# Performance work log

Hardware: AMD Instinct MI355X
Metric: run time of the kernel (lower is better)

The kernel has to match this reference:

```python
import jax, jax.numpy as jnp
import numpy as np

B, D, H, N, M, K = 128, 256, 4, 256, 256, 10  # M=256 is hardcoded in the original repeat(1,1,1,256)
DIM = D // H  # per-head dim = 64


def setup_inputs() -> dict:
    key = jax.random.key(0)
    ks = jax.random.split(key, 10)
    s = 0.05  # weight scale
    return {
        "x": jax.random.normal(ks[0], (B, D, N), jnp.float32),
        "source": jax.random.normal(ks[1], (B, D, M), jnp.float32),
        "Wq": jax.random.normal(ks[2], (D, D), jnp.float32) * s,
        "bq": jax.random.normal(ks[3], (D,), jnp.float32) * s,
        "Wk": jax.random.normal(ks[4], (D, D), jnp.float32) * s,
        "bk": jax.random.normal(ks[5], (D,), jnp.float32) * s,
        "Wv": jax.random.normal(ks[6], (D, D), jnp.float32) * s,
        "bv": jax.random.normal(ks[7], (D,), jnp.float32) * s,
        "Wm": jax.random.normal(ks[8], (D, D), jnp.float32) * s,
        "bm": jax.random.normal(ks[9], (D,), jnp.float32) * s,
        "k": K,
    }


def _pointwise(W, b, x):
    # nn.Conv1d(d, d, kernel_size=1): per-point linear over channel dim
    return jnp.einsum('ef,bfn->ben', W, x) + b[None, :, None]


def reference(x, source, Wq, bq, Wk, bk, Wv, bv, Wm, bm, k):
    b, d, n = x.shape
    # torch .view(b, dim, heads, -1) splits channels as (dim, heads)
    q = _pointwise(Wq, bq, x).reshape(b, DIM, H, n)
    kk = _pointwise(Wk, bk, source).reshape(b, DIM, H, -1)
    v = _pointwise(Wv, bv, source).reshape(b, DIM, H, -1)

    scores = jnp.einsum('bdhn,bdhm->bhnm', q, kk) / jnp.sqrt(jnp.asarray(DIM, x.dtype))
    # per-row top-k threshold: keep only scores >= k-th largest, softmax over kept
    thresh = jax.lax.top_k(scores, k)[0][..., k - 1:k]  # [b,h,n,1]
    mask = scores >= thresh
    neg = jnp.finfo(scores.dtype).min
    prob = jax.nn.softmax(jnp.where(mask, scores, neg), axis=-1)
    prob = jnp.where(mask, prob, jnp.zeros((), scores.dtype))

    out = jnp.einsum('bhnm,bdhm->bdhn', prob, v).reshape(b, d, n)
    return _pointwise(Wm, bm, out)
```

## Files before the change

kernel.cpp:

```cpp
#include <hip/hip_runtime.h>
#include <hip/hip_bf16.h>

#define BB   128
#define DDIM 256
#define HH   4
#define NNN  256
#define MMM  256

typedef __hip_bfloat16 bf16;
typedef short  short8   __attribute__((ext_vector_type(8)));
typedef unsigned short ushort8_t __attribute__((ext_vector_type(8)));
typedef float  f32x4    __attribute__((ext_vector_type(4)));
typedef float  f32x2    __attribute__((ext_vector_type(2)));

__device__ __forceinline__ unsigned short f2bf(float x) {
    unsigned u = __builtin_bit_cast(unsigned, x);
    u += 0x7FFFu + ((u >> 16) & 1u);
    return (unsigned short)(u >> 16);
}
__device__ __forceinline__ float bf2f(unsigned short b) {
    unsigned u = ((unsigned)b) << 16;
    return __builtin_bit_cast(float, u);
}

__device__ __forceinline__ void xpose4(float v[4], const int p) {
    float ta = __shfl_xor((p & 1) ? v[0] : v[1], 1, 64);
    float tb = __shfl_xor((p & 1) ? v[2] : v[3], 1, 64);
    float u0 = (p & 1) ? ta : v[0];
    float u1 = (p & 1) ? v[1] : ta;
    float u2 = (p & 1) ? tb : v[2];
    float u3 = (p & 1) ? v[3] : tb;
    float tc = __shfl_xor((p & 2) ? u0 : u2, 2, 64);
    float td = __shfl_xor((p & 2) ? u1 : u3, 2, 64);
    v[0] = (p & 2) ? tc : u0;
    v[1] = (p & 2) ? td : u1;
    v[2] = (p & 2) ? u2 : tc;
    v[3] = (p & 2) ? u3 : td;
}

__device__ __forceinline__ void split3_store8k(char* dst, const float v[4]) {
    unsigned short h[4], m[4], l[4];
    #pragma unroll
    for (int i = 0; i < 4; ++i) {
        h[i] = f2bf(v[i]);
        float r1 = v[i] - bf2f(h[i]);
        m[i] = f2bf(r1);
        float r2 = r1 - bf2f(m[i]);
        l[i] = f2bf(r2);
    }
    uint2 hp, mp, lp;
    hp.x = (unsigned)h[0] | ((unsigned)h[1] << 16);
    hp.y = (unsigned)h[2] | ((unsigned)h[3] << 16);
    mp.x = (unsigned)m[0] | ((unsigned)m[1] << 16);
    mp.y = (unsigned)m[2] | ((unsigned)m[3] << 16);
    lp.x = (unsigned)l[0] | ((unsigned)l[1] << 16);
    lp.y = (unsigned)l[2] | ((unsigned)l[3] << 16);
    *(uint2*)dst = hp;
    *(uint2*)(dst + 8192) = mp;
    *(uint2*)(dst + 16384) = lp;
}

__device__ __forceinline__ void split2_store(char* dst, const float v[4]) {
    unsigned short h[4], m[4];
    #pragma unroll
    for (int i = 0; i < 4; ++i) {
        h[i] = f2bf(v[i]);
        float r1 = v[i] - bf2f(h[i]);
        m[i] = f2bf(r1);
    }
    uint2 hp, mp;
    hp.x = (unsigned)h[0] | ((unsigned)h[1] << 16);
    hp.y = (unsigned)h[2] | ((unsigned)h[3] << 16);
    mp.x = (unsigned)m[0] | ((unsigned)m[1] << 16);
    mp.y = (unsigned)m[2] | ((unsigned)m[3] << 16);
    *(uint2*)dst = hp;
    *(uint2*)(dst + 16384) = mp;
}

__device__ __forceinline__ void ldx4(const float* p, float v[4]) {
    const float4 f = *(const float4*)p;
    v[0] = f.x; v[1] = f.y; v[2] = f.z; v[3] = f.w;
}
__device__ __forceinline__ void ldx4(const bf16* p, float v[4]) {
    uint2 u = *(const uint2*)p;
    v[0] = bf2f((unsigned short)(u.x & 0xFFFF));
    v[1] = bf2f((unsigned short)(u.x >> 16));
    v[2] = bf2f((unsigned short)(u.y & 0xFFFF));
    v[3] = bf2f((unsigned short)(u.y >> 16));
}

__device__ __forceinline__ float max16v(const float* w) {
    float a = fmaxf(fmaxf(w[0], w[1]),  fmaxf(w[2], w[3]));
    float b = fmaxf(fmaxf(w[4], w[5]),  fmaxf(w[6], w[7]));
    float c = fmaxf(fmaxf(w[8], w[9]),  fmaxf(w[10], w[11]));
    float d = fmaxf(fmaxf(w[12], w[13]), fmaxf(w[14], w[15]));
    return fmaxf(fmaxf(a, b), fmaxf(c, d));
}
__device__ __forceinline__ float gmax16(float v) {
    v = fmaxf(v, __shfl_xor(v, 1, 64));
    v = fmaxf(v, __shfl_xor(v, 2, 64));
    v = fmaxf(v, __shfl_xor(v, 4, 64));
    v = fmaxf(v, __shfl_xor(v, 8, 64));
    return v;
}
__device__ __forceinline__ float gsum16(float v) {
    v += __shfl_xor(v, 1, 64);
    v += __shfl_xor(v, 2, 64);
    v += __shfl_xor(v, 4, 64);
    v += __shfl_xor(v, 8, 64);
    return v;
}

template <int MODE>
__global__ __launch_bounds__(256)
void projqk_kernel(const float* __restrict__ X, const float* __restrict__ W,
                   const float* __restrict__ bias, float* __restrict__ Yt,
                   unsigned short* __restrict__ Ph, unsigned short* __restrict__ Pm,
                   unsigned short* __restrict__ Pl) {
    __shared__ float Wt[32][268];
    __shared__ float Xt[32][36];

    const int t  = threadIdx.x;
    const int tx = t & 7;
    const int ty = t >> 3;
    const int n0 = blockIdx.x * 32;
    const int b  = blockIdx.y;
    const size_t plane = (size_t)b * DDIM * NNN;

    f32x2 acc2[8][2];
    #pragma unroll
    for (int i = 0; i < 8; ++i) {
        acc2[i][0] = f32x2{0.f, 0.f};
        acc2[i][1] = f32x2{0.f, 0.f};
    }

    for (int f0 = 0; f0 < DDIM; f0 += 32) {
        #pragma unroll
        for (int i = 0; i < 8; ++i) {
            int idx = t + i * 256;
            int fq = idx & 7, el = idx >> 3;
            const float4 w4 = *(const float4*)&W[(size_t)el * DDIM + f0 + fq * 4];
            Wt[fq * 4 + 0][el] = w4.x;
            Wt[fq * 4 + 1][el] = w4.y;
            Wt[fq * 4 + 2][el] = w4.z;
            Wt[fq * 4 + 3][el] = w4.w;
        }
        #pragma unroll
        for (int i = 0; i < 4; ++i) {
            int idx = t + i * 256;
            int fl = idx >> 5, nl = idx & 31;
            Xt[fl][nl] = X[plane + (size_t)(f0 + fl) * NNN + n0 + nl];
        }
        __syncthreads();

        #pragma unroll
        for (int ff = 0; ff < 32; ++ff) {
            const float4 av0 = *(const float4*)&Wt[ff][ty * 8];
            const float4 av1 = *(const float4*)&Wt[ff][ty * 8 + 4];
            const float4 bv  = *(const float4*)&Xt[ff][tx * 4];
            const float a[8] = {av0.x, av0.y, av0.z, av0.w, av1.x, av1.y, av1.z, av1.w};
            const f32x2 c0 = {bv.x, bv.y};
            const f32x2 c1 = {bv.z, bv.w};
            #pragma unroll
            for (int i2 = 0; i2 < 8; ++i2) {
                const f32x2 aa = {a[i2], a[i2]};
                acc2[i2][0] = __builtin_elementwise_fma(aa, c0, acc2[i2][0]);
                acc2[i2][1] = __builtin_elementwise_fma(aa, c1, acc2[i2][1]);
            }
        }
        __syncthreads();
    }

    float* stage = &Wt[0][0];
    #pragma unroll
    for (int i2 = 0; i2 < 8; ++i2) {
        const int e = ty * 8 + i2;
        const float bs = bias[e];
        const int col = (e & 3) * 64 + (e >> 2);
        stage[(tx * 4 + 0) * 260 + col] = acc2[i2][0].x + bs;
        stage[(tx * 4 + 1) * 260 + col] = acc2[i2][0].y + bs;
        stage[(tx * 4 + 2) * 260 + col] = acc2[i2][1].x + bs;
        stage[(tx * 4 + 3) * 260 + col] = acc2[i2][1].y + bs;
    }
    __syncthreads();

    #pragma unroll
    for (int it = 0; it < 8; ++it) {
        int gid = t + it * 256;
        int n   = gid >> 6;
        int sub = gid & 63;
        const float4 v4 = *(const float4*)&stage[n * 260 + sub * 4];
        const int hh = sub >> 4;
        const int dd0 = (sub & 15) * 4;
        const size_t off = ((size_t)(b * 4 + hh) * NNN + n0 + n) * 64 + dd0;
        if constexpr (MODE == 0) {
            *(float4*)&Yt[off] = v4;
        } else {
            const float v[4] = {v4.x, v4.y, v4.z, v4.w};
            unsigned short h[4], m[4], l[4];
            #pragma unroll
            for (int i = 0; i < 4; ++i) {
                h[i] = f2bf(v[i]);
                float r1 = v[i] - bf2f(h[i]);
                m[i] = f2bf(r1);
                float r2 = r1 - bf2f(m[i]);
                l[i] = f2bf(r2);
            }
            uint2 hp, mp, lp;
            hp.x = (unsigned)h[0] | ((unsigned)h[1] << 16);
            hp.y = (unsigned)h[2] | ((unsigned)h[3] << 16);
            mp.x = (unsigned)m[0] | ((unsigned)m[1] << 16);
            mp.y = (unsigned)m[2] | ((unsigned)m[3] << 16);
            lp.x = (unsigned)l[0] | ((unsigned)l[1] << 16);
            lp.y = (unsigned)l[2] | ((unsigned)l[3] << 16);
            *(uint2*)&Ph[off] = hp;
            *(uint2*)&Pm[off] = mp;
            *(uint2*)&Pl[off] = lp;
        }
    }
}

__global__ __launch_bounds__(256, 4)
void attn4_kernel(const float* __restrict__ qt,
                  const unsigned short* __restrict__ khp,
                  const unsigned short* __restrict__ kmp,
                  const unsigned short* __restrict__ klp,
                  const bf16* __restrict__ vb, bf16* __restrict__ ob,
                  const int* __restrict__ kptr) {
    extern __shared__ __align__(16) char smem[];

    const int t    = threadIdx.x;
    const int lane = t & 63;
    const int w    = t >> 6;
    const int g    = lane >> 4;
    const int c16  = lane & 15;

    const int i    = blockIdx.x;
    const int work = (i & 7) * 256 + (i >> 3);
    const int bx = work & 3;
    const int h  = (work >> 2) & 3;
    const int b  = work >> 4;
    const int n0 = bx * 64;
    const int bh = b * 4 + h;

    const size_t planeV = (size_t)b * DDIM * MMM;

    int kk = kptr[0];
    kk = kk < 1 ? 1 : (kk > MMM ? MMM : kk);

    #pragma unroll
    for (int it = 0; it < 4; ++it) {
        int gid = t + it * 256;
        int dq = gid & 15;
        int n  = gid >> 4;
        const float4 q4 = *(const float4*)&qt[((size_t)bh * NNN + n0 + n) * 64 + dq * 4];
        float v[4] = {q4.x * 0.125f, q4.y * 0.125f, q4.z * 0.125f, q4.w * 0.125f};
        int base = n * 128 + ((dq * 8) ^ ((n & 7) << 4));
        split3_store8k(smem + base, v);
    }
    __syncthreads();

    short8 qh[2], qm[2], ql[2];
    #pragma unroll
    for (int ks = 0; ks < 2; ++ks) {
        int nl = w * 16 + c16;
        int off = nl * 128 + ((ks * 64 + g * 16) ^ ((nl & 7) << 4));
        qh[ks] = *(const short8*)(smem + off);
        qm[ks] = *(const short8*)(smem + 8192 + off);
        ql[ks] = *(const short8*)(smem + 16384 + off);
    }
    __syncthreads();

    f32x4 acc[16];
    #pragma unroll
    for (int m = 0; m < 16; ++m) acc[m] = f32x4{0.f, 0.f, 0.f, 0.f};

    #pragma unroll
    for (int tt = 0; tt < 4; ++tt) {
        if (tt) __syncthreads();
        #pragma unroll
        for (int it = 0; it < 6; ++it) {
            int gid = t + it * 256;
            int pl  = gid >> 9;
            int rem = gid & 511;
            int ml  = rem >> 3;
            int dq  = rem & 7;
            int dqs = dq ^ (ml & 7);
            const unsigned short* kp = (pl == 0) ? khp : (pl == 1 ? kmp : klp);
            const unsigned short* src = kp + ((size_t)bh * MMM + tt * 64 + ml) * 64 + dqs * 8;
            __builtin_amdgcn_global_load_lds(
                (const __attribute__((address_space(1))) void*)src,
                (__attribute__((address_space(3))) void*)(smem + gid * 16),
                16, 0, 0);
        }
        __syncthreads();

        #pragma unroll
        for (int mf = 0; mf < 4; ++mf) {
            #pragma unroll
            for (int ks = 0; ks < 2; ++ks) {
                int ml = mf * 16 + c16;
                int off = ml * 128 + ((ks * 64 + g * 16) ^ ((ml & 7) << 4));
                short8 bh_ = *(const short8*)(smem + off);
                short8 bm_ = *(const short8*)(smem + 8192 + off);
                short8 bl_ = *(const short8*)(smem + 16384 + off);
                f32x4 a = acc[tt * 4 + mf];
                a = __builtin_amdgcn_mfma_f32_16x16x32_bf16(qh[ks], bh_, a, 0, 0, 0);
                a = __builtin_amdgcn_mfma_f32_16x16x32_bf16(qh[ks], bm_, a, 0, 0, 0);
                a = __builtin_amdgcn_mfma_f32_16x16x32_bf16(qm[ks], bh_, a, 0, 0, 0);
                a = __builtin_amdgcn_mfma_f32_16x16x32_bf16(qm[ks], bm_, a, 0, 0, 0);
                a = __builtin_amdgcn_mfma_f32_16x16x32_bf16(qh[ks], bl_, a, 0, 0, 0);
                a = __builtin_amdgcn_mfma_f32_16x16x32_bf16(ql[ks], bh_, a, 0, 0, 0);
                acc[tt * 4 + mf] = a;
            }
        }
    }
    __syncthreads();

    float thr[4], rmx[4];
    #pragma unroll
    for (int r = 0; r < 4; ++r) {
        float w16[16];
        #pragma unroll
        for (int mf = 0; mf < 16; ++mf) w16[mf] = acc[mf][r];
        float lm = max16v(w16);
        float gm = gmax16(lm);
        rmx[r] = gm;
        for (int it = 1; it < kk; ++it) {
            unsigned long long bal = __ballot(lm == gm);
            unsigned gmask = (unsigned)((bal >> (g * 16)) & 0xFFFFull);
            int leader = __builtin_ctz(gmask);
            bool skip = (c16 != leader);
            #pragma unroll
            for (int mf = 0; mf < 16; ++mf) {
                bool hit = (!skip) && (w16[mf] == gm);
                w16[mf] = hit ? -INFINITY : w16[mf];
                skip = skip || hit;
            }
            lm = max16v(w16);
            gm = gmax16(lm);
        }
        thr[r] = gm;
    }

    #pragma unroll
    for (int mf = 0; mf < 16; ++mf) {
        #pragma unroll
        for (int r = 0; r < 4; ++r) {
            float a = acc[mf][r];
            acc[mf][r] = (a >= thr[r]) ? __expf(a - rmx[r]) : 0.f;
        }
    }
    float inv_[4];
    #pragma unroll
    for (int r = 0; r < 4; ++r) {
        float s = ((acc[0][r] + acc[1][r]) + (acc[2][r] + acc[3][r]))
                + ((acc[4][r] + acc[5][r]) + (acc[6][r] + acc[7][r]))
                + ((acc[8][r] + acc[9][r]) + (acc[10][r] + acc[11][r]))
                + ((acc[12][r] + acc[13][r]) + (acc[14][r] + acc[15][r]));
        s = gsum16(s);
        inv_[r] = 1.0f / s;
    }
    #pragma unroll
    for (int mf = 0; mf < 16; ++mf) {
        #pragma unroll
        for (int r = 0; r < 4; ++r) {
            int row = w * 16 + g * 4 + r;
            int m2  = (mf * 16 + c16) * 2;
            int off = row * 512 + (m2 ^ ((row & 7) << 4));
            *(unsigned short*)(smem + off) = f2bf(acc[mf][r] * inv_[r]);
        }
    }
    __syncthreads();

    f32x4 o[4];
    #pragma unroll
    for (int df = 0; df < 4; ++df) o[df] = f32x4{0.f, 0.f, 0.f, 0.f};

    #pragma unroll
    for (int half = 0; half < 2; ++half) {
        short8 pa[4];
        #pragma unroll
        for (int ks = 0; ks < 4; ++ks) {
            int row = w * 16 + c16;
            int off = row * 512 + ((half * 256 + ks * 64 + g * 16) ^ ((row & 7) << 4));
            pa[ks] = *(const short8*)(smem + off);
        }
        #pragma unroll
        for (int df = 0; df < 4; ++df) {
            int d = df * 16 + c16;
            const bf16* vrow = vb + planeV + (size_t)(d * HH + h) * MMM + half * 128;
            f32x4 o_ = o[df];
            #pragma unroll
            for (int ks = 0; ks < 4; ++ks) {
                short8 vv = *(const short8*)(vrow + ks * 32 + g * 8);
                o_ = __builtin_amdgcn_mfma_f32_16x16x32_bf16(pa[ks], vv, o_, 0, 0, 0);
            }
            o[df] = o_;
        }
    }
    __syncthreads();

    #pragma unroll
    for (int df = 0; df < 4; ++df)
        #pragma unroll
        for (int r = 0; r < 4; ++r) {
            int d  = df * 16 + c16;
            int nl = w * 16 + g * 4 + r;
            int off = d * 128 + ((nl * 2) ^ ((d & 7) << 4));
            *(unsigned short*)(smem + off) = f2bf(o[df][r]);
        }
    __syncthreads();
    #pragma unroll
    for (int it = 0; it < 2; ++it) {
        int idx = t + it * 256;
        int d = idx >> 3, ch = idx & 7;
        int off = d * 128 + ((ch * 16) ^ ((d & 7) << 4));
        ushort8_t val = *(const ushort8_t*)(smem + off);
        *(ushort8_t*)&ob[planeV + (size_t)(d * HH + h) * NNN + n0 + ch * 8] = val;
    }
}

template <typename TIN, typename TOUT>
__global__ __launch_bounds__(512, 2)
void projm_kernel(const TIN* __restrict__ X, const float* __restrict__ W,
                  const float* __restrict__ bias, TOUT* __restrict__ Y) {
    extern __shared__ __align__(16) char smem[];

    const int t    = threadIdx.x;
    const int lane = t & 63;
    const int w    = t >> 6;
    const int c16  = lane & 15;
    const int g    = (lane >> 4) & 3;
    const int p    = lane & 3;
    const int G    = lane >> 2;

    const int n0 = blockIdx.x * 128;
    const int e0 = blockIdx.y * 128;
    const int b  = blockIdx.z;
    const size_t plane = (size_t)b * DDIM * NNN;

    f32x4 acc[8];
    #pragma unroll
    for (int nf = 0; nf < 8; ++nf) acc[nf] = f32x4{0.f, 0.f, 0.f, 0.f};

    #pragma unroll
    for (int ft = 0; ft < 4; ++ft) {
        const int f0 = ft * 64;
        if (ft) __syncthreads();
        #pragma unroll
        for (int it = 0; it < 4; ++it) {
            int chunk = w + 8 * it;
            int fch = chunk & 15, nh = chunk >> 4;
            float v[4];
            ldx4(&X[plane + (size_t)(f0 + fch * 4 + p) * NNN + n0 + nh * 64 + G * 4], v);
            xpose4(v, p);
            int nl = nh * 64 + G * 4 + p;
            int base = nl * 128 + ((fch * 8) ^ ((nl & 7) << 4));
            split2_store(smem + base, v);
        }
        #pragma unroll
        for (int it = 0; it < 4; ++it) {
            int idx = t + 512 * it;
            int el = idx >> 4, fq = idx & 15;
            float v[4];
            const float4 f4 = *(const float4*)&W[(size_t)(e0 + el) * DDIM + f0 + fq * 4];
            v[0] = f4.x; v[1] = f4.y; v[2] = f4.z; v[3] = f4.w;
            int base = 32768 + el * 128 + ((fq * 8) ^ ((el & 7) << 4));
            split2_store(smem + base, v);
        }
        __syncthreads();

        const int ew = w * 16;
        short8 a0[2], a1[2];
        #pragma unroll
        for (int ks = 0; ks < 2; ++ks) {
            int off = 32768 + (ew + c16) * 128
                    + ((ks * 64 + g * 16) ^ ((c16 & 7) << 4));
            a0[ks] = *(const short8*)(smem + off);
            a1[ks] = *(const short8*)(smem + off + 16384);
        }
        #pragma unroll
        for (int nf = 0; nf < 8; ++nf) {
            #pragma unroll
            for (int ks = 0; ks < 2; ++ks) {
                int off = (nf * 16 + c16) * 128
                        + ((ks * 64 + g * 16) ^ ((c16 & 7) << 4));
                short8 b0 = *(const short8*)(smem + off);
                short8 b1 = *(const short8*)(smem + off + 16384);
                f32x4 a = acc[nf];
                a = __builtin_amdgcn_mfma_f32_16x16x32_bf16(a0[ks], b0, a, 0, 0, 0);
                a = __builtin_amdgcn_mfma_f32_16x16x32_bf16(a0[ks], b1, a, 0, 0, 0);
                a = __builtin_amdgcn_mfma_f32_16x16x32_bf16(a1[ks], b0, a, 0, 0, 0);
                acc[nf] = a;
            }
        }
    }

    const int ew = w * 16;
    float bs[4];
    #pragma unroll
    for (int r = 0; r < 4; ++r) bs[r] = bias[e0 + ew + g * 4 + r];
    #pragma unroll
    for (int nf = 0; nf < 8; ++nf) {
        #pragma unroll
        for (int r = 0; r < 4; ++r) {
            size_t off = plane + (size_t)(e0 + ew + g * 4 + r) * NNN + n0 + nf * 16 + c16;
            float val = acc[nf][r] + bs[r];
            if constexpr (sizeof(TOUT) == 4) Y[off] = val;
            else                             *(unsigned short*)&Y[off] = f2bf(val);
        }
    }
}

extern "C" void kernel_launch(void* const* d_in, const int* in_sizes, int n_in,
                              void* d_out, int out_size, void* d_ws, size_t ws_size,
                              hipStream_t stream) {
    const float* x   = (const float*)d_in[0];
    const float* src = (const float*)d_in[1];
    const float* Wq  = (const float*)d_in[2];
    const float* bq  = (const float*)d_in[3];
    const float* Wk  = (const float*)d_in[4];
    const float* bk  = (const float*)d_in[5];
    const float* Wv  = (const float*)d_in[6];
    const float* bv  = (const float*)d_in[7];
    const float* Wm  = (const float*)d_in[8];
    const float* bm  = (const float*)d_in[9];
    const int*   kp  = (const int*)d_in[10];
    float* out = (float*)d_out;

    char* ws = (char*)d_ws;
    const size_t QT_BYTES = 33554432;
    const size_t PL_BYTES = 16777216;

    float*          qt = (float*)(ws);
    unsigned short* kh = (unsigned short*)(ws + QT_BYTES);
    unsigned short* km = (unsigned short*)(ws + QT_BYTES + PL_BYTES);
    unsigned short* kl = (unsigned short*)(ws + QT_BYTES + 2 * PL_BYTES);
    bf16*           vb = (bf16*)(ws + QT_BYTES + 3 * PL_BYTES);
    bf16*           ob = (bf16*)(ws + QT_BYTES + 4 * PL_BYTES);

    hipFuncSetAttribute((const void*)(projm_kernel<float, bf16>),
                        hipFuncAttributeMaxDynamicSharedMemorySize, 65536);
    hipFuncSetAttribute((const void*)(projm_kernel<bf16, float>),
                        hipFuncAttributeMaxDynamicSharedMemorySize, 65536);
    hipFuncSetAttribute((const void*)attn4_kernel,
                        hipFuncAttributeMaxDynamicSharedMemorySize, 32768);

    dim3 qk_grid(NNN / 32, BB);
    dim3 mgrid(2, 2, BB);

    hipLaunchKernelGGL((projqk_kernel<0>), qk_grid, dim3(256), 0, stream,
                       x,   Wq, bq, qt, nullptr, nullptr, nullptr);
    hipLaunchKernelGGL((projqk_kernel<1>), qk_grid, dim3(256), 0, stream,
                       src, Wk, bk, nullptr, kh, km, kl);
    hipLaunchKernelGGL((projm_kernel<float, bf16>), mgrid, dim3(512), 65536, stream,
                       src, Wv, bv, vb);
    hipLaunchKernelGGL(attn4_kernel, dim3(2048), dim3(256), 32768, stream,
                       qt, kh, km, kl, vb, ob, kp);
    hipLaunchKernelGGL((projm_kernel<bf16, float>), mgrid, dim3(512), 65536, stream,
                       ob, Wm, bm, out);
}
```

Measured before the change: 289.9 us.

## Retile Q/K projection, drop redundant split term for bf16 input in output projection

Retiles the fp32 Q/K projection kernel from 256x32 tiles to 128x128 output tiles per block, giving more register reuse per shared-memory load and moving shared memory to dynamic allocation. The output projection with bf16 input no longer splits the input into high and low bf16 parts, since the low part is always zero. This removes one MFMA and one LDS read per step and shrinks shared memory. It also raises the attention kernel's occupancy hint to 5 and restructures max16v. The larger Q/K tiles use more registers per thread, which may limit occupancy.

```diff
diff --git a/kernel.cpp b/kernel.cpp
--- a/kernel.cpp
+++ b/kernel.cpp
@@ -77,6 +77,13 @@
     *(uint2*)(dst + 16384) = mp;
 }
 
+__device__ __forceinline__ void split1_store(char* dst, const float v[4]) {
+    uint2 hp;
+    hp.x = (unsigned)f2bf(v[0]) | ((unsigned)f2bf(v[1]) << 16);
+    hp.y = (unsigned)f2bf(v[2]) | ((unsigned)f2bf(v[3]) << 16);
+    *(uint2*)dst = hp;
+}
+
 __device__ __forceinline__ void ldx4(const float* p, float v[4]) {
     const float4 f = *(const float4*)p;
     v[0] = f.x; v[1] = f.y; v[2] = f.z; v[3] = f.w;
@@ -90,11 +97,14 @@
 }
 
 __device__ __forceinline__ float max16v(const float* w) {
-    float a = fmaxf(fmaxf(w[0], w[1]),  fmaxf(w[2], w[3]));
-    float b = fmaxf(fmaxf(w[4], w[5]),  fmaxf(w[6], w[7]));
-    float c = fmaxf(fmaxf(w[8], w[9]),  fmaxf(w[10], w[11]));
-    float d = fmaxf(fmaxf(w[12], w[13]), fmaxf(w[14], w[15]));
-    return fmaxf(fmaxf(a, b), fmaxf(c, d));
+    float a = fmaxf(fmaxf(w[0],  w[1]),  w[2]);
+    float b = fmaxf(fmaxf(w[3],  w[4]),  w[5]);
+    float c = fmaxf(fmaxf(w[6],  w[7]),  w[8]);
+    float d = fmaxf(fmaxf(w[9],  w[10]), w[11]);
+    float e = fmaxf(fmaxf(w[12], w[13]), w[14]);
+    float ab = fmaxf(fmaxf(a, b), c);
+    float de = fmaxf(fmaxf(d, e), w[15]);
+    return fmaxf(ab, de);
 }
 __device__ __forceinline__ float gmax16(float v) {
     v = fmaxf(v, __shfl_xor(v, 1, 64));
@@ -112,57 +122,62 @@
 }
 
 template <int MODE>
-__global__ __launch_bounds__(256)
+__global__ __launch_bounds__(256, 4)
 void projqk_kernel(const float* __restrict__ X, const float* __restrict__ W,
                    const float* __restrict__ bias, float* __restrict__ Yt,
                    unsigned short* __restrict__ Ph, unsigned short* __restrict__ Pm,
                    unsigned short* __restrict__ Pl) {
-    __shared__ float Wt[32][268];
-    __shared__ float Xt[32][36];
+    extern __shared__ __align__(16) char smem[];
+    float* Wt = (float*)smem;
+    float* Xt = (float*)(smem + 16896);
+    float* sbuf = (float*)smem;
 
     const int t  = threadIdx.x;
-    const int tx = t & 7;
-    const int ty = t >> 3;
-    const int n0 = blockIdx.x * 32;
-    const int b  = blockIdx.y;
+    const int tx = t & 31;
+    const int ty = t >> 5;
+    const int n0 = blockIdx.x * 128;
+    const int e0 = blockIdx.y * 128;
+    const int b  = blockIdx.z;
     const size_t plane = (size_t)b * DDIM * NNN;
 
-    f32x2 acc2[8][2];
-    #pragma unroll
-    for (int i = 0; i < 8; ++i) {
+    f32x2 acc2[16][2];
+    #pragma unroll
+    for (int i = 0; i < 16; ++i) {
         acc2[i][0] = f32x2{0.f, 0.f};
         acc2[i][1] = f32x2{0.f, 0.f};
     }
 
     for (int f0 = 0; f0 < DDIM; f0 += 32) {
         #pragma unroll
-        for (int i = 0; i < 8; ++i) {
+        for (int i = 0; i < 16; ++i) {
             int idx = t + i * 256;
-            int fq = idx & 7, el = idx >> 3;
-            const float4 w4 = *(const float4*)&W[(size_t)el * DDIM + f0 + fq * 4];
-            Wt[fq * 4 + 0][el] = w4.x;
-            Wt[fq * 4 + 1][el] = w4.y;
-            Wt[fq * 4 + 2][el] = w4.z;
-            Wt[fq * 4 + 3][el] = w4.w;
+            int fl = idx & 31, el = idx >> 5;
+            Wt[fl * 132 + el] = W[(size_t)(e0 + el) * DDIM + f0 + fl];
         }
         #pragma unroll
         for (int i = 0; i < 4; ++i) {
             int idx = t + i * 256;
-            int fl = idx >> 5, nl = idx & 31;
-            Xt[fl][nl] = X[plane + (size_t)(f0 + fl) * NNN + n0 + nl];
+            int fl = idx >> 5, nl4 = idx & 31;
+            *(float4*)&Xt[fl * 132 + nl4 * 4] =
+                *(const float4*)&X[plane + (size_t)(f0 + fl) * NNN + n0 + nl4 * 4];
         }
         __syncthreads();
 
         #pragma unroll
         for (int ff = 0; ff < 32; ++ff) {
-            const float4 av0 = *(const float4*)&Wt[ff][ty * 8];
-            const float4 av1 = *(const float4*)&Wt[ff][ty * 8 + 4];
-            const float4 bv  = *(const float4*)&Xt[ff][tx * 4];
-            const float a[8] = {av0.x, av0.y, av0.z, av0.w, av1.x, av1.y, av1.z, av1.w};
+            const float4 av0 = *(const float4*)&Wt[ff * 132 + ty * 16];
+            const float4 av1 = *(const float4*)&Wt[ff * 132 + ty * 16 + 4];
+            const float4 av2 = *(const float4*)&Wt[ff * 132 + ty * 16 + 8];
+            const float4 av3 = *(const float4*)&Wt[ff * 132 + ty * 16 + 12];
+            const float4 bv  = *(const float4*)&Xt[ff * 132 + tx * 4];
+            const float a[16] = {av0.x, av0.y, av0.z, av0.w,
+                                 av1.x, av1.y, av1.z, av1.w,
+                                 av2.x, av2.y, av2.z, av2.w,
+                                 av3.x, av3.y, av3.z, av3.w};
             const f32x2 c0 = {bv.x, bv.y};
             const f32x2 c1 = {bv.z, bv.w};
             #pragma unroll
-            for (int i2 = 0; i2 < 8; ++i2) {
+            for (int i2 = 0; i2 < 16; ++i2) {
                 const f32x2 aa = {a[i2], a[i2]};
                 acc2[i2][0] = __builtin_elementwise_fma(aa, c0, acc2[i2][0]);
                 acc2[i2][1] = __builtin_elementwise_fma(aa, c1, acc2[i2][1]);
@@ -171,56 +186,67 @@
         __syncthreads();
     }
 
-    float* stage = &Wt[0][0];
-    #pragma unroll
-    for (int i2 = 0; i2 < 8; ++i2) {
-        const int e = ty * 8 + i2;
-        const float bs = bias[e];
-        const int col = (e & 3) * 64 + (e >> 2);
-        stage[(tx * 4 + 0) * 260 + col] = acc2[i2][0].x + bs;
-        stage[(tx * 4 + 1) * 260 + col] = acc2[i2][0].y + bs;
-        stage[(tx * 4 + 2) * 260 + col] = acc2[i2][1].x + bs;
-        stage[(tx * 4 + 3) * 260 + col] = acc2[i2][1].y + bs;
-    }
-    __syncthreads();
-
-    #pragma unroll
-    for (int it = 0; it < 8; ++it) {
-        int gid = t + it * 256;
-        int n   = gid >> 6;
-        int sub = gid & 63;
-        const float4 v4 = *(const float4*)&stage[n * 260 + sub * 4];
-        const int hh = sub >> 4;
-        const int dd0 = (sub & 15) * 4;
-        const size_t off = ((size_t)(b * 4 + hh) * NNN + n0 + n) * 64 + dd0;
-        if constexpr (MODE == 0) {
-            *(float4*)&Yt[off] = v4;
-        } else {
-            const float v[4] = {v4.x, v4.y, v4.z, v4.w};
-            unsigned short h[4], m[4], l[4];
+    float bsv[16];
+    #pragma unroll
+    for (int i2 = 0; i2 < 16; ++i2) bsv[i2] = bias[e0 + ty * 16 + i2];
+
+    #pragma unroll
+    for (int hf = 0; hf < 2; ++hf) {
+        if ((tx >> 4) == hf) {
             #pragma unroll
-            for (int i = 0; i < 4; ++i) {
-                h[i] = f2bf(v[i]);
-                float r1 = v[i] - bf2f(h[i]);
-                m[i] = f2bf(r1);
-                float r2 = r1 - bf2f(m[i]);
-                l[i] = f2bf(r2);
-            }
-            uint2 hp, mp, lp;
-            hp.x = (unsigned)h[0] | ((unsigned)h[1] << 16);
-            hp.y = (unsigned)h[2] | ((unsigned)h[3] << 16);
-            mp.x = (unsigned)m[0] | ((unsigned)m[1] << 16);
-            mp.y = (unsigned)m[2] | ((unsigned)m[3] << 16);
-            lp.x = (unsigned)l[0] | ((unsigned)l[1] << 16);
-            lp.y = (unsigned)l[2] | ((unsigned)l[3] << 16);
-            *(uint2*)&Ph[off] = hp;
-            *(uint2*)&Pm[off] = mp;
-            *(uint2*)&Pl[off] = lp;
-        }
-    }
-}
-
-__global__ __launch_bounds__(256, 4)
+            for (int i2 = 0; i2 < 16; ++i2) {
+                const int e = e0 + ty * 16 + i2;
+                const int col = (e & 3) * 32 + ((e >> 2) - (e0 >> 2));
+                const float vals[4] = {acc2[i2][0].x + bsv[i2], acc2[i2][0].y + bsv[i2],
+                                       acc2[i2][1].x + bsv[i2], acc2[i2][1].y + bsv[i2]};
+                const int nb = (tx - hf * 16) * 4;
+                sbuf[(nb + 0) * 132 + col] = vals[0];
+                sbuf[(nb + 1) * 132 + col] = vals[1];
+                sbuf[(nb + 2) * 132 + col] = vals[2];
+                sbuf[(nb + 3) * 132 + col] = vals[3];
+            }
+        }
+        __syncthreads();
+        #pragma unroll
+        for (int it = 0; it < 8; ++it) {
+            int u  = t + it * 256;
+            int c4 = u & 31;
+            int n  = u >> 5;
+            const float4 v4 = *(const float4*)&sbuf[n * 132 + c4 * 4];
+            const int hh = c4 >> 3;
+            const int dq = c4 & 7;
+            const size_t off = ((size_t)(b * 4 + hh) * NNN + n0 + hf * 64 + n) * 64
+                             + (e0 >> 2) + dq * 4;
+            if constexpr (MODE == 0) {
+                *(float4*)&Yt[off] = v4;
+            } else {
+                const float v[4] = {v4.x, v4.y, v4.z, v4.w};
+                unsigned short h[4], m[4], l[4];
+                #pragma unroll
+                for (int i = 0; i < 4; ++i) {
+                    h[i] = f2bf(v[i]);
+                    float r1 = v[i] - bf2f(h[i]);
+                    m[i] = f2bf(r1);
+                    float r2 = r1 - bf2f(m[i]);
+                    l[i] = f2bf(r2);
+                }
+                uint2 hp, mp, lp;
+                hp.x = (unsigned)h[0] | ((unsigned)h[1] << 16);
+                hp.y = (unsigned)h[2] | ((unsigned)h[3] << 16);
+                mp.x = (unsigned)m[0] | ((unsigned)m[1] << 16);
+                mp.y = (unsigned)m[2] | ((unsigned)m[3] << 16);
+                lp.x = (unsigned)l[0] | ((unsigned)l[1] << 16);
+                lp.y = (unsigned)l[2] | ((unsigned)l[3] << 16);
+                *(uint2*)&Ph[off] = hp;
+                *(uint2*)&Pm[off] = mp;
+                *(uint2*)&Pl[off] = lp;
+            }
+        }
+        __syncthreads();
+    }
+}
+
+__global__ __launch_bounds__(256, 5)
 void attn4_kernel(const float* __restrict__ qt,
                   const unsigned short* __restrict__ khp,
                   const unsigned short* __restrict__ kmp,
@@ -426,6 +452,8 @@
 void projm_kernel(const TIN* __restrict__ X, const float* __restrict__ W,
                   const float* __restrict__ bias, TOUT* __restrict__ Y) {
     extern __shared__ __align__(16) char smem[];
+    constexpr bool XBF = (sizeof(TIN) == 2);
+    constexpr int WOFF = XBF ? 16384 : 32768;
 
     const int t    = threadIdx.x;
     const int lane = t & 63;
@@ -457,7 +485,8 @@
             xpose4(v, p);
             int nl = nh * 64 + G * 4 + p;
             int base = nl * 128 + ((fch * 8) ^ ((nl & 7) << 4));
-            split2_store(smem + base, v);
+            if constexpr (XBF) split1_store(smem + base, v);
+            else               split2_store(smem + base, v);
         }
         #pragma unroll
         for (int it = 0; it < 4; ++it) {
@@ -466,7 +495,7 @@
             float v[4];
             const float4 f4 = *(const float4*)&W[(size_t)(e0 + el) * DDIM + f0 + fq * 4];
             v[0] = f4.x; v[1] = f4.y; v[2] = f4.z; v[3] = f4.w;
-            int base = 32768 + el * 128 + ((fq * 8) ^ ((el & 7) << 4));
+            int base = WOFF + el * 128 + ((fq * 8) ^ ((el & 7) << 4));
             split2_store(smem + base, v);
         }
         __syncthreads();
@@ -475,7 +504,7 @@
         short8 a0[2], a1[2];
         #pragma unroll
         for (int ks = 0; ks < 2; ++ks) {
-            int off = 32768 + (ew + c16) * 128
+            int off = WOFF + (ew + c16) * 128
                     + ((ks * 64 + g * 16) ^ ((c16 & 7) << 4));
             a0[ks] = *(const short8*)(smem + off);
             a1[ks] = *(const short8*)(smem + off + 16384);
@@ -487,10 +516,12 @@
                 int off = (nf * 16 + c16) * 128
                         + ((ks * 64 + g * 16) ^ ((c16 & 7) << 4));
                 short8 b0 = *(const short8*)(smem + off);
-                short8 b1 = *(const short8*)(smem + off + 16384);
                 f32x4 a = acc[nf];
                 a = __builtin_amdgcn_mfma_f32_16x16x32_bf16(a0[ks], b0, a, 0, 0, 0);
-                a = __builtin_amdgcn_mfma_f32_16x16x32_bf16(a0[ks], b1, a, 0, 0, 0);
+                if constexpr (!XBF) {
+                    short8 b1 = *(const short8*)(smem + off + 16384);
+                    a = __builtin_amdgcn_mfma_f32_16x16x32_bf16(a0[ks], b1, a, 0, 0, 0);
+                }
                 a = __builtin_amdgcn_mfma_f32_16x16x32_bf16(a1[ks], b0, a, 0, 0, 0);
                 acc[nf] = a;
             }
@@ -540,24 +571,28 @@
     bf16*           vb = (bf16*)(ws + QT_BYTES + 3 * PL_BYTES);
     bf16*           ob = (bf16*)(ws + QT_BYTES + 4 * PL_BYTES);
 
+    hipFuncSetAttribute((const void*)(projqk_kernel<0>),
+                        hipFuncAttributeMaxDynamicSharedMemorySize, 33792);
+    hipFuncSetAttribute((const void*)(projqk_kernel<1>),
+                        hipFuncAttributeMaxDynamicSharedMemorySize, 33792);
     hipFuncSetAttribute((const void*)(projm_kernel<float, bf16>),
                         hipFuncAttributeMaxDynamicSharedMemorySize, 65536);
     hipFuncSetAttribute((const void*)(projm_kernel<bf16, float>),
-                        hipFuncAttributeMaxDynamicSharedMemorySize, 65536);
+                        hipFuncAttributeMaxDynamicSharedMemorySize, 49152);
     hipFuncSetAttribute((const void*)attn4_kernel,
                         hipFuncAttributeMaxDynamicSharedMemorySize, 32768);
 
-    dim3 qk_grid(NNN / 32, BB);
+    dim3 qk_grid(NNN / 128, DDIM / 128, BB);
     dim3 mgrid(2, 2, BB);
 
-    hipLaunchKernelGGL((projqk_kernel<0>), qk_grid, dim3(256), 0, stream,
+    hipLaunchKernelGGL((projqk_kernel<0>), qk_grid, dim3(256), 33792, stream,
                        x,   Wq, bq, qt, nullptr, nullptr, nullptr);
-    hipLaunchKernelGGL((projqk_kernel<1>), qk_grid, dim3(256), 0, stream,
+    hipLaunchKernelGGL((projqk_kernel<1>), qk_grid, dim3(256), 33792, stream,
                        src, Wk, bk, nullptr, kh, km, kl);
     hipLaunchKernelGGL((projm_kernel<float, bf16>), mgrid, dim3(512), 65536, stream,
                        src, Wv, bv, vb);
     hipLaunchKernelGGL(attn4_kernel, dim3(2048), dim3(256), 32768, stream,
                        qt, kh, km, kl, vb, ob, kp);
-    hipLaunchKernelGGL((projm_kernel<bf16, float>), mgrid, dim3(512), 65536, stream,
+    hipLaunchKernelGGL((projm_kernel<bf16, float>), mgrid, dim3(512), 49152, stream,
                        ob, Wm, bm, out);
 }
```

After: 351.9 us. +21.4%, slower.
